# Kernel optimization log

Measured on AMD Instinct MI355X. Metric: run time of the kernel, lower is better.

Reference implementation:

```python
import jax, jax.numpy as jnp
import numpy as np

SIGMA = 2.5
NEIGH_THRESH = 8.0
COORD_SCALE = 40.0  # Angstrom-scale box so the 8A cutoff gives realistic sparsity


def _rbf_weights(vs, vg):
    # vs: [B, Ns, 3], vg: [B, Ng, 3] -> [B, Ns, Ng] row-normalized gaussian RBF
    d2 = (jnp.sum(vs * vs, -1)[:, :, None]
          + jnp.sum(vg * vg, -1)[:, None, :]
          - 2.0 * jnp.einsum('bnd,bmd->bnm', vs, vg))
    d2 = jnp.maximum(d2, 0.0)
    w = jnp.exp(-d2 / (SIGMA ** 2)) * (d2 < NEIGH_THRESH ** 2)
    return w / (jnp.sum(w, -1, keepdims=True) + 1e-8)


def setup_inputs() -> dict:
    key = jax.random.key(0)
    ks = jax.random.split(key, 12)
    B, Ns, Ng, D = 4, 16384, 2048, 128
    s = 1.0 / np.sqrt(D)
    sp = 1.0 / np.sqrt(2 * D)
    return {
        'xs': jax.random.normal(ks[0], (B, Ns, D), jnp.float32),
        'xg': jax.random.normal(ks[1], (B, Ng, D), jnp.float32),
        'vs': jax.random.uniform(ks[2], (B, Ns, 3), jnp.float32) * COORD_SCALE,
        'vg': jax.random.uniform(ks[3], (B, Ng, 3), jnp.float32) * COORD_SCALE,
        'Ws_pre': jax.random.normal(ks[4], (D, D), jnp.float32) * s,
        'bs_pre': jnp.zeros((D,), jnp.float32),
        'Wg_pre': jax.random.normal(ks[5], (D, D), jnp.float32) * s,
        'bg_pre': jnp.zeros((D,), jnp.float32),
        'Ws_post': jax.random.normal(ks[6], (2 * D, D), jnp.float32) * sp,
        'bs_post': jnp.zeros((D,), jnp.float32),
        'Wg_post': jax.random.normal(ks[7], (2 * D, D), jnp.float32) * sp,
        'bg_post': jnp.zeros((D,), jnp.float32),
    }


def reference(xs, xg, vs, vg, Ws_pre, bs_pre, Wg_pre, bg_pre,
              Ws_post, bs_post, Wg_post, bg_post):
    # pre-encoders (surface.x = s_pre_block(surface.x); graph.x = g_pre_block(graph.x))
    xs_h = jax.nn.relu(jnp.einsum('bnd,de->bne', xs, Ws_pre) + bs_pre)
    xg_h = jax.nn.relu(jnp.einsum('bmd,de->bme', xg, Wg_pre) + bg_pre)
    # RBF bipartite message passing (non-BP path): xs_out = rbf_w @ graph.x; xg_out = rbf_w.T @ surface.x
    w = _rbf_weights(vs, vg)                                  # [B, Ns, Ng]
    xs_out = jnp.einsum('bnm,bmd->bnd', w, xg_h)              # graph -> surface
    xg_out = jnp.einsum('bnm,bnd->bmd', w, xs_h)              # surface -> graph
    # post blocks fuse old features with messages
    xs_new = jax.nn.relu(jnp.einsum('bnd,de->bne',
                                    jnp.concatenate([xs_h, xs_out], -1), Ws_post) + bs_post)
    xg_new = jax.nn.relu(jnp.einsum('bmd,de->bme',
                                    jnp.concatenate([xg_h, xg_out], -1), Wg_post) + bg_post)
    # concat along node dim so output is a single array: [B, Ns+Ng, D]
    return jnp.concatenate([xs_new, xg_new], axis=1)
```

## Files before the change

### kernel.cpp

```cpp
#include <hip/hip_runtime.h>
#include <hip/hip_bf16.h>

#define BB 4
#define NS 16384
#define NG 2048
#define DD 128
#define SPLITG 16
#define C2F (-0.23083120f)

typedef short bf16x8 __attribute__((ext_vector_type(8)));
typedef unsigned short u16x8 __attribute__((ext_vector_type(8)));
typedef float f32x4 __attribute__((ext_vector_type(4)));
typedef float f32x16 __attribute__((ext_vector_type(16)));
typedef int i32x4 __attribute__((ext_vector_type(4)));

#if __has_builtin(__builtin_amdgcn_exp2f)
#define EXP2(x) __builtin_amdgcn_exp2f(x)
#else
#define EXP2(x) exp2f(x)
#endif

__device__ __forceinline__ unsigned short f2bf(float x) {
  unsigned int u = __builtin_bit_cast(unsigned int, x);
  u += 0x7FFFu + ((u >> 16) & 1u);
  return (unsigned short)(u >> 16);
}
__device__ __forceinline__ float bf2f(unsigned short h) {
  unsigned int u = ((unsigned int)h) << 16;
  return __builtin_bit_cast(float, u);
}

#define PACK_SWAP(e0, e1, e2, e3, e4, e5, e6, e7, OUT)                        \
  {                                                                           \
    unsigned pq0, pq1, pq2, pq3;                                              \
    asm("v_cvt_pk_bf16_f32 %0, %4, %5\n\t"                                    \
        "v_cvt_pk_bf16_f32 %1, %6, %7\n\t"                                    \
        "v_cvt_pk_bf16_f32 %2, %8, %9\n\t"                                    \
        "v_cvt_pk_bf16_f32 %3, %10, %11\n\t"                                  \
        "s_nop 1\n\t"                                                         \
        "v_permlane32_swap_b32 %0, %2\n\t"                                    \
        "v_permlane32_swap_b32 %1, %3\n\t"                                    \
        "s_nop 1"                                                             \
        : "=&v"(pq0), "=&v"(pq1), "=&v"(pq2), "=&v"(pq3)                      \
        : "v"(e0), "v"(e1), "v"(e2), "v"(e3), "v"(e4), "v"(e5), "v"(e6),      \
          "v"(e7));                                                           \
    i32x4 tmp_ = {(int)pq0, (int)pq1, (int)pq2, (int)pq3};                    \
    OUT = __builtin_bit_cast(bf16x8, tmp_);                                   \
  }

__device__ __forceinline__ void posprep1(const float* __restrict__ v, int i,
                                         unsigned short* __restrict__ pos1,
                                         unsigned short* __restrict__ pos2) {
  float x = v[i * 3 + 0], y = v[i * 3 + 1], z = v[i * 3 + 2];
  unsigned short hx = f2bf(x), hy = f2bf(y), hz = f2bf(z);
  float fx = bf2f(hx), fy = bf2f(hy), fz = bf2f(hz);
  unsigned short lx = f2bf(x - fx), ly = f2bf(y - fy), lz = f2bf(z - fz);
  float n = x * x + y * y + z * z;
  unsigned short nh = f2bf(n);
  unsigned short nl = f2bf(n - bf2f(nh));
  unsigned short m2hx = f2bf(-2.f * fx), m2hy = f2bf(-2.f * fy),
                 m2hz = f2bf(-2.f * fz);
  unsigned short m2lx = f2bf(-2.f * bf2f(lx)), m2ly = f2bf(-2.f * bf2f(ly)),
                 m2lz = f2bf(-2.f * bf2f(lz));
  const unsigned short one = 0x3F80;
  u16x8 a0 = {m2hx, m2hy, m2hz, m2lx, m2ly, m2lz, m2hx, m2hy};
  u16x8 a1 = {m2hz, m2lx, m2ly, m2lz, nh, nl, one, one};
  u16x8 b0 = {hx, hy, hz, hx, hy, hz, lx, ly};
  u16x8 b1 = {lz, lx, ly, lz, one, one, nh, nl};
  *(u16x8*)(pos1 + (long)i * 16) = a0;
  *(u16x8*)(pos1 + (long)i * 16 + 8) = a1;
  *(u16x8*)(pos2 + (long)i * 16) = b0;
  *(u16x8*)(pos2 + (long)i * 16 + 8) = b1;
}

__global__ __launch_bounds__(256) void prep_k(
    const float* __restrict__ vs, const float* __restrict__ vg,
    const float* __restrict__ Ws_pre, const float* __restrict__ Wg_pre,
    const float* __restrict__ Ws_post, const float* __restrict__ Wg_post,
    unsigned short* __restrict__ pos1_s, unsigned short* __restrict__ pos2_s,
    unsigned short* __restrict__ pos1_g, unsigned short* __restrict__ pos2_g,
    unsigned short* __restrict__ WtS_pre, unsigned short* __restrict__ WtG_pre,
    unsigned short* __restrict__ WtS_post,
    unsigned short* __restrict__ WtG_post) {
  const int NODEBLK = (BB * (NS + NG)) / 256;
  int bid = blockIdx.x, tid = threadIdx.x;
  if (bid < NODEBLK) {
    int i = bid * 256 + tid;
    if (i < BB * NS)
      posprep1(vs, i, pos1_s, pos2_s);
    else
      posprep1(vg, i - BB * NS, pos1_g, pos2_g);
  } else {
    int k2 = (bid - NODEBLK) * 256 + tid;
    const float* W;
    unsigned short* Wt;
    int kshift, loc;
    if (k2 < 16384) { W = Ws_pre; Wt = WtS_pre; kshift = 7; loc = k2; }
    else if (k2 < 32768) { W = Wg_pre; Wt = WtG_pre; kshift = 7; loc = k2 - 16384; }
    else if (k2 < 65536) { W = Ws_post; Wt = WtS_post; kshift = 8; loc = k2 - 32768; }
    else { W = Wg_post; Wt = WtG_post; kshift = 8; loc = k2 - 65536; }
    int K = 1 << kshift;
    int e = loc >> kshift, k = loc & (K - 1);
    Wt[(long)e * K + k] = f2bf(W[(long)k * 128 + e]);
  }
}

__global__ __launch_bounds__(256) void pre_mfma_k(
    const float* __restrict__ xs, const float* __restrict__ xg,
    const unsigned short* __restrict__ WtS,
    const unsigned short* __restrict__ WtG, const float* __restrict__ bs,
    const float* __restrict__ bg, unsigned short* __restrict__ xs_h,
    unsigned short* __restrict__ xg_h) {
  long r0 = (long)blockIdx.x * 64;
  const float* X;
  const unsigned short* Wt;
  const float* bias;
  unsigned short* H;
  long row0;
  if (r0 < (long)BB * NS) {
    X = xs; Wt = WtS; bias = bs; H = xs_h; row0 = r0;
  } else {
    X = xg; Wt = WtG; bias = bg; H = xg_h; row0 = r0 - (long)BB * NS;
  }
  int tid = threadIdx.x, l = tid & 63, w = tid >> 6;
  int g = l >> 4, r = l & 15;
  row0 += w * 16;
  const float* xrow = X + (row0 + r) * DD;
  f32x4 z4 = {0.f, 0.f, 0.f, 0.f};
  f32x4 acc[8];
#pragma unroll
  for (int i = 0; i < 8; ++i) acc[i] = z4;
#pragma unroll
  for (int ks = 0; ks < 4; ++ks) {
    float4 v0 = *(const float4*)(xrow + ks * 32 + 8 * g);
    float4 v1 = *(const float4*)(xrow + ks * 32 + 8 * g + 4);
    bf16x8 a;
    a[0] = (short)f2bf(v0.x); a[1] = (short)f2bf(v0.y);
    a[2] = (short)f2bf(v0.z); a[3] = (short)f2bf(v0.w);
    a[4] = (short)f2bf(v1.x); a[5] = (short)f2bf(v1.y);
    a[6] = (short)f2bf(v1.z); a[7] = (short)f2bf(v1.w);
#pragma unroll
    for (int ct = 0; ct < 8; ++ct) {
      bf16x8 b = *reinterpret_cast<const bf16x8*>(Wt + (ct * 16 + r) * DD +
                                                  ks * 32 + 8 * g);
      acc[ct] = __builtin_amdgcn_mfma_f32_16x16x32_bf16(a, b, acc[ct], 0, 0, 0);
    }
  }
#pragma unroll
  for (int ct = 0; ct < 8; ++ct) {
    float bv = bias[ct * 16 + r];
#pragma unroll
    for (int r4 = 0; r4 < 4; ++r4) {
      long row = row0 + 4 * g + r4;
      H[row * DD + ct * 16 + r] = f2bf(fmaxf(acc[ct][r4] + bv, 0.f));
    }
  }
}

__global__ __launch_bounds__(256) void transpose_k(
    const unsigned short* __restrict__ H, unsigned short* __restrict__ HT,
    int R, const float* __restrict__ scale) {
  __shared__ unsigned short lds[64 * 136];
  int tid = threadIdx.x;
  long r0 = (long)blockIdx.x * 64;
#pragma unroll
  for (int q = 0; q < 4; ++q) {
    int idx = q * 2048 + tid * 8;
    int rr = idx >> 7, cc = idx & 127;
    u16x8 v = *reinterpret_cast<const u16x8*>(H + (r0 + rr) * 128 + cc);
    if (scale) {
      float s = scale[r0 + rr];
#pragma unroll
      for (int i = 0; i < 8; ++i) v[i] = f2bf(bf2f(v[i]) * s);
    }
    *(u16x8*)&lds[rr * 136 + cc] = v;
  }
  __syncthreads();
  int e = tid >> 1, half = tid & 1;
#pragma unroll
  for (int q = 0; q < 4; ++q) {
    u16x8 v;
#pragma unroll
    for (int i = 0; i < 8; ++i)
      v[i] = lds[(half * 32 + q * 8 + i) * 136 + e];
    *reinterpret_cast<u16x8*>(HT + (long)e * R + r0 + half * 32 + q * 8) = v;
  }
}

__global__ __launch_bounds__(256) void msg_s_k(
    const unsigned short* __restrict__ pos1_g,
    const unsigned short* __restrict__ pos2_s,
    const unsigned short* __restrict__ xg_hT, unsigned short* __restrict__ xs_o,
    float* __restrict__ rsinv) {
  __shared__ __align__(16) unsigned short ldsB[2][128 * 64];
  const int tid = threadIdx.x;
  const int w = tid >> 6, l = tid & 63;
  const int ln = l & 31, hi = l >> 5;
  const int b = blockIdx.y;
  const long bNS = (long)b * NS, bNG = (long)b * NG;
  const long row0 = (long)blockIdx.x * 128 + w * 32;
  const long BNG = (long)BB * NG;
  const int NCH = NG / 64;

  const bf16x8 bP = *reinterpret_cast<const bf16x8*>(
      pos2_s + (bNS + row0 + ln) * 16 + 8 * hi);

  const f32x16 zz = {0.f, 0.f, 0.f, 0.f, 0.f, 0.f, 0.f, 0.f,
                     0.f, 0.f, 0.f, 0.f, 0.f, 0.f, 0.f, 0.f};
  f32x16 acc[4] = {zz, zz, zz, zz};
  float rs0 = 0.f, rs1 = 0.f, rs2 = 0.f, rs3 = 0.f;

  const int tf = tid >> 3;
  const int tsp = tid & 7;
  const unsigned short* p0 = xg_hT + (long)tf * BNG + bNG + (tsp ^ (tf & 7)) * 8;
  const unsigned short* p1 = p0 + (long)32 * BNG;
  const unsigned short* p2 = p0 + (long)64 * BNG;
  const unsigned short* p3 = p0 + (long)96 * BNG;
  const unsigned short* pp = pos1_g + (bNG + ln) * 16 + 8 * hi;

  u16x8 stA[4];
  bf16x8 pA0, pA1, pA0n, pA1n;
  stA[0] = *reinterpret_cast<const u16x8*>(p0);
  stA[1] = *reinterpret_cast<const u16x8*>(p1);
  stA[2] = *reinterpret_cast<const u16x8*>(p2);
  stA[3] = *reinterpret_cast<const u16x8*>(p3);
#pragma unroll
  for (int q = 0; q < 4; ++q)
    *(u16x8*)&ldsB[0][(q * 32 + tf) * 64 + tsp * 8] = stA[q];
  stA[0] = *reinterpret_cast<const u16x8*>(p0 + 64);
  stA[1] = *reinterpret_cast<const u16x8*>(p1 + 64);
  stA[2] = *reinterpret_cast<const u16x8*>(p2 + 64);
  stA[3] = *reinterpret_cast<const u16x8*>(p3 + 64);
  p0 += 128; p1 += 128; p2 += 128; p3 += 128;
  pA0 = *reinterpret_cast<const bf16x8*>(pp);
  pA1 = *reinterpret_cast<const bf16x8*>(pp + 32 * 16);
  pA0n = *reinterpret_cast<const bf16x8*>(pp + 64 * 16);
  pA1n = *reinterpret_cast<const bf16x8*>(pp + 96 * 16);
  pp += 128 * 16;
  __syncthreads();

#pragma unroll 1
  for (int c = 0; c < NCH; ++c) {
    const int buf = c & 1;
    float ex[2][16];
    bf16x8 fr[2][2];
    f32x16 S0 = __builtin_amdgcn_mfma_f32_32x32x16_bf16(pA0, bP, zz, 0, 0, 0);
    f32x16 S1 = __builtin_amdgcn_mfma_f32_32x32x16_bf16(pA1, bP, zz, 0, 0, 0);
#pragma unroll
    for (int r = 0; r < 16; ++r) ex[0][r] = EXP2(S0[r] * C2F);
    PACK_SWAP(ex[0][0], ex[0][1], ex[0][2], ex[0][3], ex[0][4], ex[0][5],
              ex[0][6], ex[0][7], fr[0][0]);
    PACK_SWAP(ex[0][8], ex[0][9], ex[0][10], ex[0][11], ex[0][12], ex[0][13],
              ex[0][14], ex[0][15], fr[0][1]);
#pragma unroll
    for (int r = 0; r < 16; ++r) ex[1][r] = EXP2(S1[r] * C2F);
    PACK_SWAP(ex[1][0], ex[1][1], ex[1][2], ex[1][3], ex[1][4], ex[1][5],
              ex[1][6], ex[1][7], fr[1][0]);
    PACK_SWAP(ex[1][8], ex[1][9], ex[1][10], ex[1][11], ex[1][12], ex[1][13],
              ex[1][14], ex[1][15], fr[1][1]);
#pragma unroll
    for (int r = 0; r < 4; ++r) {
      rs0 += ex[0][r] + ex[1][r];
      rs1 += ex[0][r + 4] + ex[1][r + 4];
      rs2 += ex[0][r + 8] + ex[1][r + 8];
      rs3 += ex[0][r + 12] + ex[1][r + 12];
    }
#pragma unroll
    for (int t2 = 0; t2 < 2; ++t2) {
#pragma unroll
      for (int kh = 0; kh < 2; ++kh) {
        const int kt = t2 * 2 + kh;
        const int spr = ((kt * 2 + hi) ^ (ln & 7)) * 8;
#pragma unroll
        for (int nt = 0; nt < 4; ++nt) {
          const bf16x8 bm = *reinterpret_cast<const bf16x8*>(
              &ldsB[buf][(nt * 32 + ln) * 64 + spr]);
          acc[nt] = __builtin_amdgcn_mfma_f32_32x32x16_bf16(fr[t2][kh], bm,
                                                            acc[nt], 0, 0, 0);
        }
      }
    }
    if (c + 1 < NCH) {
#pragma unroll
      for (int q = 0; q < 4; ++q)
        *(u16x8*)&ldsB[buf ^ 1][(q * 32 + tf) * 64 + tsp * 8] = stA[q];
    }
    if (c + 2 < NCH) {
      stA[0] = *reinterpret_cast<const u16x8*>(p0);
      stA[1] = *reinterpret_cast<const u16x8*>(p1);
      stA[2] = *reinterpret_cast<const u16x8*>(p2);
      stA[3] = *reinterpret_cast<const u16x8*>(p3);
      p0 += 64; p1 += 64; p2 += 64; p3 += 64;
    }
    pA0 = pA0n;
    pA1 = pA1n;
    if (c + 2 < NCH) {
      pA0n = *reinterpret_cast<const bf16x8*>(pp);
      pA1n = *reinterpret_cast<const bf16x8*>(pp + 32 * 16);
      pp += 64 * 16;
    }
    __syncthreads();
  }

  float rtot = (rs0 + rs1) + (rs2 + rs3);
  rtot += __shfl_xor(rtot, 32, 64);
  float denom = rtot + 1e-8f;
  float rsi = 1.f / denom;
  if (hi == 0) rsinv[bNS + row0 + ln] = rsi;
#pragma unroll
  for (int r = 0; r < 16; ++r) {
    const int crow = (r & 3) + 8 * (r >> 2) + 4 * hi;
    float rsib = __shfl(rsi, crow, 64);
    long rowg = bNS + row0 + crow;
#pragma unroll
    for (int nt = 0; nt < 4; ++nt)
      xs_o[rowg * DD + nt * 32 + ln] = f2bf(acc[nt][r] * rsib);
  }
}

__global__ __launch_bounds__(256) void msg_g_k(
    const unsigned short* __restrict__ pos1_s,
    const unsigned short* __restrict__ pos2_g,
    const unsigned short* __restrict__ xs_hT, unsigned short* __restrict__ part) {
  __shared__ __align__(16) unsigned short ldsB[2][128 * 64];
  const int tid = threadIdx.x;
  const int w = tid >> 6, l = tid & 63;
  const int ln = l & 31, hi = l >> 5;
  const int b = blockIdx.y, spz = blockIdx.z;
  const long bNS = (long)b * NS, bNG = (long)b * NG;
  const long nbeg = (long)spz * (NS / SPLITG);
  const long row0 = (long)blockIdx.x * 128 + w * 32;
  const long BNS = (long)BB * NS;
  const int NCH = (NS / SPLITG) / 64;

  const bf16x8 bP = *reinterpret_cast<const bf16x8*>(
      pos2_g + (bNG + row0 + ln) * 16 + 8 * hi);

  const f32x16 zz = {0.f, 0.f, 0.f, 0.f, 0.f, 0.f, 0.f, 0.f,
                     0.f, 0.f, 0.f, 0.f, 0.f, 0.f, 0.f, 0.f};
  f32x16 acc[4] = {zz, zz, zz, zz};

  const int tf = tid >> 3;
  const int tsp = tid & 7;
  const unsigned short* p0 = xs_hT + (long)tf * BNS + bNS + nbeg +
                             (tsp ^ (tf & 7)) * 8;
  const unsigned short* p1 = p0 + (long)32 * BNS;
  const unsigned short* p2 = p0 + (long)64 * BNS;
  const unsigned short* p3 = p0 + (long)96 * BNS;
  const unsigned short* pp = pos1_s + (bNS + nbeg + ln) * 16 + 8 * hi;

  u16x8 stA[4];
  bf16x8 pA0, pA1, pA0n, pA1n;
  stA[0] = *reinterpret_cast<const u16x8*>(p0);
  stA[1] = *reinterpret_cast<const u16x8*>(p1);
  stA[2] = *reinterpret_cast<const u16x8*>(p2);
  stA[3] = *reinterpret_cast<const u16x8*>(p3);
#pragma unroll
  for (int q = 0; q < 4; ++q)
    *(u16x8*)&ldsB[0][(q * 32 + tf) * 64 + tsp * 8] = stA[q];
  stA[0] = *reinterpret_cast<const u16x8*>(p0 + 64);
  stA[1] = *reinterpret_cast<const u16x8*>(p1 + 64);
  stA[2] = *reinterpret_cast<const u16x8*>(p2 + 64);
  stA[3] = *reinterpret_cast<const u16x8*>(p3 + 64);
  p0 += 128; p1 += 128; p2 += 128; p3 += 128;
  pA0 = *reinterpret_cast<const bf16x8*>(pp);
  pA1 = *reinterpret_cast<const bf16x8*>(pp + 32 * 16);
  pA0n = *reinterpret_cast<const bf16x8*>(pp + 64 * 16);
  pA1n = *reinterpret_cast<const bf16x8*>(pp + 96 * 16);
  pp += 128 * 16;
  __syncthreads();

#pragma unroll 1
  for (int c = 0; c < NCH; ++c) {
    const int buf = c & 1;
    float ex[2][16];
    bf16x8 fr[2][2];
    f32x16 S0 = __builtin_amdgcn_mfma_f32_32x32x16_bf16(pA0, bP, zz, 0, 0, 0);
    f32x16 S1 = __builtin_amdgcn_mfma_f32_32x32x16_bf16(pA1, bP, zz, 0, 0, 0);
#pragma unroll
    for (int r = 0; r < 16; ++r) ex[0][r] = EXP2(S0[r] * C2F);
    PACK_SWAP(ex[0][0], ex[0][1], ex[0][2], ex[0][3], ex[0][4], ex[0][5],
              ex[0][6], ex[0][7], fr[0][0]);
    PACK_SWAP(ex[0][8], ex[0][9], ex[0][10], ex[0][11], ex[0][12], ex[0][13],
              ex[0][14], ex[0][15], fr[0][1]);
#pragma unroll
    for (int r = 0; r < 16; ++r) ex[1][r] = EXP2(S1[r] * C2F);
    PACK_SWAP(ex[1][0], ex[1][1], ex[1][2], ex[1][3], ex[1][4], ex[1][5],
              ex[1][6], ex[1][7], fr[1][0]);
    PACK_SWAP(ex[1][8], ex[1][9], ex[1][10], ex[1][11], ex[1][12], ex[1][13],
              ex[1][14], ex[1][15], fr[1][1]);
#pragma unroll
    for (int t2 = 0; t2 < 2; ++t2) {
#pragma unroll
      for (int kh = 0; kh < 2; ++kh) {
        const int kt = t2 * 2 + kh;
        const int spr = ((kt * 2 + hi) ^ (ln & 7)) * 8;
#pragma unroll
        for (int nt = 0; nt < 4; ++nt) {
          const bf16x8 bm = *reinterpret_cast<const bf16x8*>(
              &ldsB[buf][(nt * 32 + ln) * 64 + spr]);
          acc[nt] = __builtin_amdgcn_mfma_f32_32x32x16_bf16(fr[t2][kh], bm,
                                                            acc[nt], 0, 0, 0);
        }
      }
    }
    if (c + 1 < NCH) {
#pragma unroll
      for (int q = 0; q < 4; ++q)
        *(u16x8*)&ldsB[buf ^ 1][(q * 32 + tf) * 64 + tsp * 8] = stA[q];
    }
    if (c + 2 < NCH) {
      stA[0] = *reinterpret_cast<const u16x8*>(p0);
      stA[1] = *reinterpret_cast<const u16x8*>(p1);
      stA[2] = *reinterpret_cast<const u16x8*>(p2);
      stA[3] = *reinterpret_cast<const u16x8*>(p3);
      p0 += 64; p1 += 64; p2 += 64; p3 += 64;
    }
    pA0 = pA0n;
    pA1 = pA1n;
    if (c + 2 < NCH) {
      pA0n = *reinterpret_cast<const bf16x8*>(pp);
      pA1n = *reinterpret_cast<const bf16x8*>(pp + 32 * 16);
      pp += 64 * 16;
    }
    __syncthreads();
  }

  const long pbase = (long)spz * BB * NG;
#pragma unroll
  for (int r = 0; r < 16; ++r) {
    const int crow = (r & 3) + 8 * (r >> 2) + 4 * hi;
    long rowg = pbase + bNG + row0 + crow;
#pragma unroll
    for (int nt = 0; nt < 4; ++nt)
      part[rowg * DD + nt * 32 + ln] = f2bf(acc[nt][r]);
  }
}

__global__ __launch_bounds__(256) void reduce_k(
    const unsigned short* __restrict__ part, unsigned short* __restrict__ xg_o) {
  long i = ((long)blockIdx.x * 256 + threadIdx.x) * 8;
  const long S = (long)BB * NG * DD;
  float a[8];
#pragma unroll
  for (int k = 0; k < 8; ++k) a[k] = 0.f;
#pragma unroll
  for (int s = 0; s < SPLITG; ++s) {
    u16x8 v = *reinterpret_cast<const u16x8*>(part + s * S + i);
#pragma unroll
    for (int k = 0; k < 8; ++k) a[k] += bf2f(v[k]);
  }
  u16x8 o;
#pragma unroll
  for (int k = 0; k < 8; ++k) o[k] = f2bf(a[k]);
  *reinterpret_cast<u16x8*>(xg_o + i) = o;
}

__global__ __launch_bounds__(256) void post_mfma_k(
    const unsigned short* __restrict__ Ha, const unsigned short* __restrict__ Hb,
    const unsigned short* __restrict__ Wt, const float* __restrict__ bias,
    float* __restrict__ out, int shift, int mask, int off) {
  int tid = threadIdx.x, l = tid & 63, w = tid >> 6;
  int g = l >> 4, r = l & 15;
  long row0 = (long)blockIdx.x * 64 + w * 16;
  const unsigned short* ha = Ha + (row0 + r) * DD;
  const unsigned short* hb = Hb + (row0 + r) * DD;
  f32x4 z4 = {0.f, 0.f, 0.f, 0.f};
  f32x4 acc[8];
#pragma unroll
  for (int i = 0; i < 8; ++i) acc[i] = z4;
#pragma unroll
  for (int ks = 0; ks < 8; ++ks) {
    const unsigned short* src = (ks < 4) ? (ha + ks * 32) : (hb + (ks - 4) * 32);
    bf16x8 a = *reinterpret_cast<const bf16x8*>(src + 8 * g);
#pragma unroll
    for (int ct = 0; ct < 8; ++ct) {
      bf16x8 b = *reinterpret_cast<const bf16x8*>(Wt + (ct * 16 + r) * 256 +
                                                  ks * 32 + 8 * g);
      acc[ct] = __builtin_amdgcn_mfma_f32_16x16x32_bf16(a, b, acc[ct], 0, 0, 0);
    }
  }
#pragma unroll
  for (int ct = 0; ct < 8; ++ct) {
    float bv = bias[ct * 16 + r];
#pragma unroll
    for (int r4 = 0; r4 < 4; ++r4) {
      long rowg = row0 + 4 * g + r4;
      long bb = rowg >> shift;
      long n = rowg & mask;
      out[(bb * (NS + NG) + off + n) * DD + ct * 16 + r] =
          fmaxf(acc[ct][r4] + bv, 0.f);
    }
  }
}

extern "C" void kernel_launch(void* const* d_in, const int* in_sizes, int n_in,
                              void* d_out, int out_size, void* d_ws,
                              size_t ws_size, hipStream_t stream) {
  const float* xs = (const float*)d_in[0];
  const float* xg = (const float*)d_in[1];
  const float* vs = (const float*)d_in[2];
  const float* vg = (const float*)d_in[3];
  const float* Ws_pre = (const float*)d_in[4];
  const float* bs_pre = (const float*)d_in[5];
  const float* Wg_pre = (const float*)d_in[6];
  const float* bg_pre = (const float*)d_in[7];
  const float* Ws_post = (const float*)d_in[8];
  const float* bs_post = (const float*)d_in[9];
  const float* Wg_post = (const float*)d_in[10];
  const float* bg_post = (const float*)d_in[11];
  float* out = (float*)d_out;

  char* p = (char*)d_ws;
  unsigned short* pos1_s = (unsigned short*)p; p += (size_t)BB * NS * 16 * 2;
  unsigned short* pos2_s = (unsigned short*)p; p += (size_t)BB * NS * 16 * 2;
  unsigned short* pos1_g = (unsigned short*)p; p += (size_t)BB * NG * 16 * 2;
  unsigned short* pos2_g = (unsigned short*)p; p += (size_t)BB * NG * 16 * 2;
  unsigned short* WtS_pre = (unsigned short*)p; p += (size_t)128 * 128 * 2;
  unsigned short* WtG_pre = (unsigned short*)p; p += (size_t)128 * 128 * 2;
  unsigned short* WtS_post = (unsigned short*)p; p += (size_t)128 * 256 * 2;
  unsigned short* WtG_post = (unsigned short*)p; p += (size_t)128 * 256 * 2;
  unsigned short* xg_h = (unsigned short*)p; p += (size_t)BB * NG * DD * 2;
  unsigned short* xg_hT = (unsigned short*)p; p += (size_t)BB * NG * DD * 2;
  unsigned short* xs_hT = (unsigned short*)p; p += (size_t)BB * NS * DD * 2;
  unsigned short* xg_o = (unsigned short*)p; p += (size_t)BB * NG * DD * 2;
  float* rsinv = (float*)p; p += (size_t)BB * NS * 4;
  unsigned short* xs_h = (unsigned short*)p;
  unsigned short* xs_o = xs_h + (size_t)BB * NS * DD;
  unsigned short* part_g = xs_h;
  p += (size_t)2 * BB * NS * DD * 2;

  prep_k<<<(BB * (NS + NG)) / 256 + 98304 / 256, 256, 0, stream>>>(
      vs, vg, Ws_pre, Wg_pre, Ws_post, Wg_post, pos1_s, pos2_s, pos1_g,
      pos2_g, WtS_pre, WtG_pre, WtS_post, WtG_post);
  pre_mfma_k<<<(BB * NS + BB * NG) / 64, 256, 0, stream>>>(
      xs, xg, WtS_pre, WtG_pre, bs_pre, bg_pre, xs_h, xg_h);
  transpose_k<<<BB * NG / 64, 256, 0, stream>>>(xg_h, xg_hT, BB * NG, nullptr);
  msg_s_k<<<dim3(NS / 128, BB), 256, 0, stream>>>(pos1_g, pos2_s, xg_hT, xs_o,
                                                  rsinv);
  transpose_k<<<BB * NS / 64, 256, 0, stream>>>(xs_h, xs_hT, BB * NS, rsinv);
  post_mfma_k<<<BB * NS / 64, 256, 0, stream>>>(xs_h, xs_o, WtS_post, bs_post,
                                                out, 14, NS - 1, 0);
  msg_g_k<<<dim3(NG / 128, BB, SPLITG), 256, 0, stream>>>(pos1_s, pos2_g,
                                                          xs_hT, part_g);
  reduce_k<<<(BB * NG * DD) / 8 / 256, 256, 0, stream>>>(part_g, xg_o);
  post_mfma_k<<<BB * NG / 64, 256, 0, stream>>>(xg_h, xg_o, WtG_post, bg_post,
                                                out, 11, NG - 1, NS);
}
```

Before: 204.1 us.

## Precompute row sums and merge both message kernels into one interleaved launch

Computes the RBF row-normalisation sums in a separate column-split rowsum kernel, so the surface-scaled transpose no longer has to wait for the surface message kernel. The graph→surface and surface→graph message GEMMs then run as alternating blocks of one 1024-block launch, giving the GPU a single larger wave of work. The graph-side split-K partials are accumulated with float atomics into a zeroed buffer plus a small convert kernel, replacing the bf16 partial buffer and the reduce kernel. The cost is recomputing the exp tile once more for the row sums, plus atomic traffic and a memset.

```diff
diff --git a/kernel.cpp b/kernel.cpp
--- a/kernel.cpp
+++ b/kernel.cpp
@@ -5,11 +5,13 @@
 #define NS 16384
 #define NG 2048
 #define DD 128
-#define SPLITG 16
+#define SPLITG 8
+#define CSPLIT 4
 #define C2F (-0.23083120f)
 
 typedef short bf16x8 __attribute__((ext_vector_type(8)));
 typedef unsigned short u16x8 __attribute__((ext_vector_type(8)));
+typedef unsigned short u16x4 __attribute__((ext_vector_type(4)));
 typedef float f32x4 __attribute__((ext_vector_type(4)));
 typedef float f32x16 __attribute__((ext_vector_type(16)));
 typedef int i32x4 __attribute__((ext_vector_type(4)));
@@ -157,9 +159,38 @@
   }
 }
 
+__global__ __launch_bounds__(256) void rowsum_k(
+    const unsigned short* __restrict__ pos1_g,
+    const unsigned short* __restrict__ pos2_s, float* __restrict__ rs_part) {
+  const int tid = threadIdx.x;
+  const int w = tid >> 6, l = tid & 63;
+  const int ln = l & 31, hi = l >> 5;
+  const int b = blockIdx.y, cz = blockIdx.z;
+  const long bNS = (long)b * NS, bNG = (long)b * NG;
+  const long row0 = (long)blockIdx.x * 128 + w * 32;
+  const int NCOL = NG / CSPLIT;
+
+  const bf16x8 bP = *reinterpret_cast<const bf16x8*>(
+      pos2_s + (bNS + row0 + ln) * 16 + 8 * hi);
+  const unsigned short* pp =
+      pos1_g + (bNG + (long)cz * NCOL + ln) * 16 + 8 * hi;
+  const f32x16 zz = {0.f, 0.f, 0.f, 0.f, 0.f, 0.f, 0.f, 0.f,
+                     0.f, 0.f, 0.f, 0.f, 0.f, 0.f, 0.f, 0.f};
+  float rsl = 0.f;
+#pragma unroll 2
+  for (int c = 0; c < NCOL / 32; ++c) {
+    bf16x8 a = *reinterpret_cast<const bf16x8*>(pp + (long)c * 32 * 16);
+    f32x16 S = __builtin_amdgcn_mfma_f32_32x32x16_bf16(a, bP, zz, 0, 0, 0);
+#pragma unroll
+    for (int r = 0; r < 16; ++r) rsl += EXP2(S[r] * C2F);
+  }
+  rsl += __shfl_xor(rsl, 32, 64);
+  if (hi == 0) rs_part[(long)cz * (BB * NS) + bNS + row0 + ln] = rsl;
+}
+
 __global__ __launch_bounds__(256) void transpose_k(
     const unsigned short* __restrict__ H, unsigned short* __restrict__ HT,
-    int R, const float* __restrict__ scale) {
+    int R, const float* __restrict__ rsp, float* __restrict__ rsinv_out) {
   __shared__ unsigned short lds[64 * 136];
   int tid = threadIdx.x;
   long r0 = (long)blockIdx.x * 64;
@@ -168,10 +199,14 @@
     int idx = q * 2048 + tid * 8;
     int rr = idx >> 7, cc = idx & 127;
     u16x8 v = *reinterpret_cast<const u16x8*>(H + (r0 + rr) * 128 + cc);
-    if (scale) {
-      float s = scale[r0 + rr];
-#pragma unroll
-      for (int i = 0; i < 8; ++i) v[i] = f2bf(bf2f(v[i]) * s);
+    if (rsp) {
+      long row = r0 + rr;
+      float s = rsp[row] + rsp[(long)BB * NS + row] +
+                rsp[2L * BB * NS + row] + rsp[3L * BB * NS + row] + 1e-8f;
+      float ri = 1.f / s;
+#pragma unroll
+      for (int i = 0; i < 8; ++i) v[i] = f2bf(bf2f(v[i]) * ri);
+      if (cc == 0) rsinv_out[row] = ri;
     }
     *(u16x8*)&lds[rr * 136 + cc] = v;
   }
@@ -187,273 +222,249 @@
   }
 }
 
-__global__ __launch_bounds__(256) void msg_s_k(
+__global__ __launch_bounds__(256) void msg_merged_k(
     const unsigned short* __restrict__ pos1_g,
     const unsigned short* __restrict__ pos2_s,
-    const unsigned short* __restrict__ xg_hT, unsigned short* __restrict__ xs_o,
-    float* __restrict__ rsinv) {
+    const unsigned short* __restrict__ xg_hT,
+    const unsigned short* __restrict__ pos1_s,
+    const unsigned short* __restrict__ pos2_g,
+    const unsigned short* __restrict__ xs_hT,
+    const float* __restrict__ rsinv, unsigned short* __restrict__ xs_o,
+    float* __restrict__ xg_acc) {
   __shared__ __align__(16) unsigned short ldsB[2][128 * 64];
   const int tid = threadIdx.x;
   const int w = tid >> 6, l = tid & 63;
   const int ln = l & 31, hi = l >> 5;
-  const int b = blockIdx.y;
-  const long bNS = (long)b * NS, bNG = (long)b * NG;
-  const long row0 = (long)blockIdx.x * 128 + w * 32;
-  const long BNG = (long)BB * NG;
-  const int NCH = NG / 64;
-
-  const bf16x8 bP = *reinterpret_cast<const bf16x8*>(
-      pos2_s + (bNS + row0 + ln) * 16 + 8 * hi);
-
+  const int bid = blockIdx.x;
+  const int role = bid & 1;
+  const int idx = bid >> 1;
   const f32x16 zz = {0.f, 0.f, 0.f, 0.f, 0.f, 0.f, 0.f, 0.f,
                      0.f, 0.f, 0.f, 0.f, 0.f, 0.f, 0.f, 0.f};
-  f32x16 acc[4] = {zz, zz, zz, zz};
-  float rs0 = 0.f, rs1 = 0.f, rs2 = 0.f, rs3 = 0.f;
-
   const int tf = tid >> 3;
   const int tsp = tid & 7;
-  const unsigned short* p0 = xg_hT + (long)tf * BNG + bNG + (tsp ^ (tf & 7)) * 8;
-  const unsigned short* p1 = p0 + (long)32 * BNG;
-  const unsigned short* p2 = p0 + (long)64 * BNG;
-  const unsigned short* p3 = p0 + (long)96 * BNG;
-  const unsigned short* pp = pos1_g + (bNG + ln) * 16 + 8 * hi;
-
-  u16x8 stA[4];
-  bf16x8 pA0, pA1, pA0n, pA1n;
-  stA[0] = *reinterpret_cast<const u16x8*>(p0);
-  stA[1] = *reinterpret_cast<const u16x8*>(p1);
-  stA[2] = *reinterpret_cast<const u16x8*>(p2);
-  stA[3] = *reinterpret_cast<const u16x8*>(p3);
-#pragma unroll
-  for (int q = 0; q < 4; ++q)
-    *(u16x8*)&ldsB[0][(q * 32 + tf) * 64 + tsp * 8] = stA[q];
-  stA[0] = *reinterpret_cast<const u16x8*>(p0 + 64);
-  stA[1] = *reinterpret_cast<const u16x8*>(p1 + 64);
-  stA[2] = *reinterpret_cast<const u16x8*>(p2 + 64);
-  stA[3] = *reinterpret_cast<const u16x8*>(p3 + 64);
-  p0 += 128; p1 += 128; p2 += 128; p3 += 128;
-  pA0 = *reinterpret_cast<const bf16x8*>(pp);
-  pA1 = *reinterpret_cast<const bf16x8*>(pp + 32 * 16);
-  pA0n = *reinterpret_cast<const bf16x8*>(pp + 64 * 16);
-  pA1n = *reinterpret_cast<const bf16x8*>(pp + 96 * 16);
-  pp += 128 * 16;
-  __syncthreads();
+
+  if (role == 0) {
+    const int b = idx >> 7;
+    const long bNS = (long)b * NS, bNG = (long)b * NG;
+    const long row0 = (long)(idx & 127) * 128 + w * 32;
+    const long BNG = (long)BB * NG;
+    const int NCH = NG / 64;
+
+    const bf16x8 bP = *reinterpret_cast<const bf16x8*>(
+        pos2_s + (bNS + row0 + ln) * 16 + 8 * hi);
+    f32x16 acc[4] = {zz, zz, zz, zz};
+
+    const unsigned short* p0 =
+        xg_hT + (long)tf * BNG + bNG + (tsp ^ (tf & 7)) * 8;
+    const unsigned short* p1 = p0 + (long)32 * BNG;
+    const unsigned short* p2 = p0 + (long)64 * BNG;
+    const unsigned short* p3 = p0 + (long)96 * BNG;
+    const unsigned short* pp = pos1_g + (bNG + ln) * 16 + 8 * hi;
+
+    u16x8 stA[4];
+    bf16x8 pA0, pA1, pA0n, pA1n;
+    stA[0] = *reinterpret_cast<const u16x8*>(p0);
+    stA[1] = *reinterpret_cast<const u16x8*>(p1);
+    stA[2] = *reinterpret_cast<const u16x8*>(p2);
+    stA[3] = *reinterpret_cast<const u16x8*>(p3);
+#pragma unroll
+    for (int q = 0; q < 4; ++q)
+      *(u16x8*)&ldsB[0][(q * 32 + tf) * 64 + tsp * 8] = stA[q];
+    stA[0] = *reinterpret_cast<const u16x8*>(p0 + 64);
+    stA[1] = *reinterpret_cast<const u16x8*>(p1 + 64);
+    stA[2] = *reinterpret_cast<const u16x8*>(p2 + 64);
+    stA[3] = *reinterpret_cast<const u16x8*>(p3 + 64);
+    p0 += 128; p1 += 128; p2 += 128; p3 += 128;
+    pA0 = *reinterpret_cast<const bf16x8*>(pp);
+    pA1 = *reinterpret_cast<const bf16x8*>(pp + 32 * 16);
+    pA0n = *reinterpret_cast<const bf16x8*>(pp + 64 * 16);
+    pA1n = *reinterpret_cast<const bf16x8*>(pp + 96 * 16);
+    pp += 128 * 16;
+    __syncthreads();
 
 #pragma unroll 1
-  for (int c = 0; c < NCH; ++c) {
-    const int buf = c & 1;
-    float ex[2][16];
-    bf16x8 fr[2][2];
-    f32x16 S0 = __builtin_amdgcn_mfma_f32_32x32x16_bf16(pA0, bP, zz, 0, 0, 0);
-    f32x16 S1 = __builtin_amdgcn_mfma_f32_32x32x16_bf16(pA1, bP, zz, 0, 0, 0);
-#pragma unroll
-    for (int r = 0; r < 16; ++r) ex[0][r] = EXP2(S0[r] * C2F);
-    PACK_SWAP(ex[0][0], ex[0][1], ex[0][2], ex[0][3], ex[0][4], ex[0][5],
-              ex[0][6], ex[0][7], fr[0][0]);
-    PACK_SWAP(ex[0][8], ex[0][9], ex[0][10], ex[0][11], ex[0][12], ex[0][13],
-              ex[0][14], ex[0][15], fr[0][1]);
-#pragma unroll
-    for (int r = 0; r < 16; ++r) ex[1][r] = EXP2(S1[r] * C2F);
-    PACK_SWAP(ex[1][0], ex[1][1], ex[1][2], ex[1][3], ex[1][4], ex[1][5],
-              ex[1][6], ex[1][7], fr[1][0]);
-    PACK_SWAP(ex[1][8], ex[1][9], ex[1][10], ex[1][11], ex[1][12], ex[1][13],
-              ex[1][14], ex[1][15], fr[1][1]);
-#pragma unroll
-    for (int r = 0; r < 4; ++r) {
-      rs0 += ex[0][r] + ex[1][r];
-      rs1 += ex[0][r + 4] + ex[1][r + 4];
-      rs2 += ex[0][r + 8] + ex[1][r + 8];
-      rs3 += ex[0][r + 12] + ex[1][r + 12];
-    }
-#pragma unroll
-    for (int t2 = 0; t2 < 2; ++t2) {
-#pragma unroll
-      for (int kh = 0; kh < 2; ++kh) {
-        const int kt = t2 * 2 + kh;
-        const int spr = ((kt * 2 + hi) ^ (ln & 7)) * 8;
-#pragma unroll
-        for (int nt = 0; nt < 4; ++nt) {
-          const bf16x8 bm = *reinterpret_cast<const bf16x8*>(
-              &ldsB[buf][(nt * 32 + ln) * 64 + spr]);
-          acc[nt] = __builtin_amdgcn_mfma_f32_32x32x16_bf16(fr[t2][kh], bm,
-                                                            acc[nt], 0, 0, 0);
+    for (int c = 0; c < NCH; ++c) {
+      const int buf = c & 1;
+      float ex[2][16];
+      bf16x8 fr[2][2];
+      f32x16 S0 = __builtin_amdgcn_mfma_f32_32x32x16_bf16(pA0, bP, zz, 0, 0, 0);
+      f32x16 S1 = __builtin_amdgcn_mfma_f32_32x32x16_bf16(pA1, bP, zz, 0, 0, 0);
+#pragma unroll
+      for (int r = 0; r < 16; ++r) ex[0][r] = EXP2(S0[r] * C2F);
+      PACK_SWAP(ex[0][0], ex[0][1], ex[0][2], ex[0][3], ex[0][4], ex[0][5],
+                ex[0][6], ex[0][7], fr[0][0]);
+      PACK_SWAP(ex[0][8], ex[0][9], ex[0][10], ex[0][11], ex[0][12], ex[0][13],
+                ex[0][14], ex[0][15], fr[0][1]);
+#pragma unroll
+      for (int r = 0; r < 16; ++r) ex[1][r] = EXP2(S1[r] * C2F);
+      PACK_SWAP(ex[1][0], ex[1][1], ex[1][2], ex[1][3], ex[1][4], ex[1][5],
+                ex[1][6], ex[1][7], fr[1][0]);
+      PACK_SWAP(ex[1][8], ex[1][9], ex[1][10], ex[1][11], ex[1][12], ex[1][13],
+                ex[1][14], ex[1][15], fr[1][1]);
+#pragma unroll
+      for (int t2 = 0; t2 < 2; ++t2) {
+#pragma unroll
+        for (int kh = 0; kh < 2; ++kh) {
+          const int kt = t2 * 2 + kh;
+          const int spr = ((kt * 2 + hi) ^ (ln & 7)) * 8;
+#pragma unroll
+          for (int nt = 0; nt < 4; ++nt) {
+            const bf16x8 bm = *reinterpret_cast<const bf16x8*>(
+                &ldsB[buf][(nt * 32 + ln) * 64 + spr]);
+            acc[nt] = __builtin_amdgcn_mfma_f32_32x32x16_bf16(fr[t2][kh], bm,
+                                                              acc[nt], 0, 0, 0);
+          }
         }
       }
-    }
-    if (c + 1 < NCH) {
-#pragma unroll
-      for (int q = 0; q < 4; ++q)
-        *(u16x8*)&ldsB[buf ^ 1][(q * 32 + tf) * 64 + tsp * 8] = stA[q];
-    }
-    if (c + 2 < NCH) {
-      stA[0] = *reinterpret_cast<const u16x8*>(p0);
-      stA[1] = *reinterpret_cast<const u16x8*>(p1);
-      stA[2] = *reinterpret_cast<const u16x8*>(p2);
-      stA[3] = *reinterpret_cast<const u16x8*>(p3);
-      p0 += 64; p1 += 64; p2 += 64; p3 += 64;
-    }
-    pA0 = pA0n;
-    pA1 = pA1n;
-    if (c + 2 < NCH) {
-      pA0n = *reinterpret_cast<const bf16x8*>(pp);
-      pA1n = *reinterpret_cast<const bf16x8*>(pp + 32 * 16);
-      pp += 64 * 16;
-    }
+      if (c + 1 < NCH) {
+#pragma unroll
+        for (int q = 0; q < 4; ++q)
+          *(u16x8*)&ldsB[buf ^ 1][(q * 32 + tf) * 64 + tsp * 8] = stA[q];
+      }
+      if (c + 2 < NCH) {
+        stA[0] = *reinterpret_cast<const u16x8*>(p0);
+        stA[1] = *reinterpret_cast<const u16x8*>(p1);
+        stA[2] = *reinterpret_cast<const u16x8*>(p2);
+        stA[3] = *reinterpret_cast<const u16x8*>(p3);
+        p0 += 64; p1 += 64; p2 += 64; p3 += 64;
+      }
+      pA0 = pA0n;
+      pA1 = pA1n;
+      if (c + 2 < NCH) {
+        pA0n = *reinterpret_cast<const bf16x8*>(pp);
+        pA1n = *reinterpret_cast<const bf16x8*>(pp + 32 * 16);
+        pp += 64 * 16;
+      }
+      __syncthreads();
+    }
+
+    float rsi = rsinv[bNS + row0 + ln];
+#pragma unroll
+    for (int r = 0; r < 16; ++r) {
+      const int crow = (r & 3) + 8 * (r >> 2) + 4 * hi;
+      float rsib = __shfl(rsi, crow, 64);
+      long rowg = bNS + row0 + crow;
+#pragma unroll
+      for (int nt = 0; nt < 4; ++nt)
+        xs_o[rowg * DD + nt * 32 + ln] = f2bf(acc[nt][r] * rsib);
+    }
+  } else {
+    const int gx = idx & 15;
+    const int b = (idx >> 4) & 3;
+    const int spz = idx >> 6;
+    const long bNS = (long)b * NS, bNG = (long)b * NG;
+    const long nbeg = (long)spz * (NS / SPLITG);
+    const long row0 = (long)gx * 128 + w * 32;
+    const long BNS = (long)BB * NS;
+    const int NCH = (NS / SPLITG) / 64;
+
+    const bf16x8 bP = *reinterpret_cast<const bf16x8*>(
+        pos2_g + (bNG + row0 + ln) * 16 + 8 * hi);
+    f32x16 acc[4] = {zz, zz, zz, zz};
+
+    const unsigned short* p0 =
+        xs_hT + (long)tf * BNS + bNS + nbeg + (tsp ^ (tf & 7)) * 8;
+    const unsigned short* p1 = p0 + (long)32 * BNS;
+    const unsigned short* p2 = p0 + (long)64 * BNS;
+    const unsigned short* p3 = p0 + (long)96 * BNS;
+    const unsigned short* pp = pos1_s + (bNS + nbeg + ln) * 16 + 8 * hi;
+
+    u16x8 stA[4];
+    bf16x8 pA0, pA1, pA0n, pA1n;
+    stA[0] = *reinterpret_cast<const u16x8*>(p0);
+    stA[1] = *reinterpret_cast<const u16x8*>(p1);
+    stA[2] = *reinterpret_cast<const u16x8*>(p2);
+    stA[3] = *reinterpret_cast<const u16x8*>(p3);
+#pragma unroll
+    for (int q = 0; q < 4; ++q)
+      *(u16x8*)&ldsB[0][(q * 32 + tf) * 64 + tsp * 8] = stA[q];
+    stA[0] = *reinterpret_cast<const u16x8*>(p0 + 64);
+    stA[1] = *reinterpret_cast<const u16x8*>(p1 + 64);
+    stA[2] = *reinterpret_cast<const u16x8*>(p2 + 64);
+    stA[3] = *reinterpret_cast<const u16x8*>(p3 + 64);
+    p0 += 128; p1 += 128; p2 += 128; p3 += 128;
+    pA0 = *reinterpret_cast<const bf16x8*>(pp);
+    pA1 = *reinterpret_cast<const bf16x8*>(pp + 32 * 16);
+    pA0n = *reinterpret_cast<const bf16x8*>(pp + 64 * 16);
+    pA1n = *reinterpret_cast<const bf16x8*>(pp + 96 * 16);
+    pp += 128 * 16;
     __syncthreads();
-  }
-
-  float rtot = (rs0 + rs1) + (rs2 + rs3);
-  rtot += __shfl_xor(rtot, 32, 64);
-  float denom = rtot + 1e-8f;
-  float rsi = 1.f / denom;
-  if (hi == 0) rsinv[bNS + row0 + ln] = rsi;
-#pragma unroll
-  for (int r = 0; r < 16; ++r) {
-    const int crow = (r & 3) + 8 * (r >> 2) + 4 * hi;
-    float rsib = __shfl(rsi, crow, 64);
-    long rowg = bNS + row0 + crow;
-#pragma unroll
-    for (int nt = 0; nt < 4; ++nt)
-      xs_o[rowg * DD + nt * 32 + ln] = f2bf(acc[nt][r] * rsib);
-  }
-}
-
-__global__ __launch_bounds__(256) void msg_g_k(
-    const unsigned short* __restrict__ pos1_s,
-    const unsigned short* __restrict__ pos2_g,
-    const unsigned short* __restrict__ xs_hT, unsigned short* __restrict__ part) {
-  __shared__ __align__(16) unsigned short ldsB[2][128 * 64];
-  const int tid = threadIdx.x;
-  const int w = tid >> 6, l = tid & 63;
-  const int ln = l & 31, hi = l >> 5;
-  const int b = blockIdx.y, spz = blockIdx.z;
-  const long bNS = (long)b * NS, bNG = (long)b * NG;
-  const long nbeg = (long)spz * (NS / SPLITG);
-  const long row0 = (long)blockIdx.x * 128 + w * 32;
-  const long BNS = (long)BB * NS;
-  const int NCH = (NS / SPLITG) / 64;
-
-  const bf16x8 bP = *reinterpret_cast<const bf16x8*>(
-      pos2_g + (bNG + row0 + ln) * 16 + 8 * hi);
-
-  const f32x16 zz = {0.f, 0.f, 0.f, 0.f, 0.f, 0.f, 0.f, 0.f,
-                     0.f, 0.f, 0.f, 0.f, 0.f, 0.f, 0.f, 0.f};
-  f32x16 acc[4] = {zz, zz, zz, zz};
-
-  const int tf = tid >> 3;
-  const int tsp = tid & 7;
-  const unsigned short* p0 = xs_hT + (long)tf * BNS + bNS + nbeg +
-                             (tsp ^ (tf & 7)) * 8;
-  const unsigned short* p1 = p0 + (long)32 * BNS;
-  const unsigned short* p2 = p0 + (long)64 * BNS;
-  const unsigned short* p3 = p0 + (long)96 * BNS;
-  const unsigned short* pp = pos1_s + (bNS + nbeg + ln) * 16 + 8 * hi;
-
-  u16x8 stA[4];
-  bf16x8 pA0, pA1, pA0n, pA1n;
-  stA[0] = *reinterpret_cast<const u16x8*>(p0);
-  stA[1] = *reinterpret_cast<const u16x8*>(p1);
-  stA[2] = *reinterpret_cast<const u16x8*>(p2);
-  stA[3] = *reinterpret_cast<const u16x8*>(p3);
-#pragma unroll
-  for (int q = 0; q < 4; ++q)
-    *(u16x8*)&ldsB[0][(q * 32 + tf) * 64 + tsp * 8] = stA[q];
-  stA[0] = *reinterpret_cast<const u16x8*>(p0 + 64);
-  stA[1] = *reinterpret_cast<const u16x8*>(p1 + 64);
-  stA[2] = *reinterpret_cast<const u16x8*>(p2 + 64);
-  stA[3] = *reinterpret_cast<const u16x8*>(p3 + 64);
-  p0 += 128; p1 += 128; p2 += 128; p3 += 128;
-  pA0 = *reinterpret_cast<const bf16x8*>(pp);
-  pA1 = *reinterpret_cast<const bf16x8*>(pp + 32 * 16);
-  pA0n = *reinterpret_cast<const bf16x8*>(pp + 64 * 16);
-  pA1n = *reinterpret_cast<const bf16x8*>(pp + 96 * 16);
-  pp += 128 * 16;
-  __syncthreads();
 
 #pragma unroll 1
-  for (int c = 0; c < NCH; ++c) {
-    const int buf = c & 1;
-    float ex[2][16];
-    bf16x8 fr[2][2];
-    f32x16 S0 = __builtin_amdgcn_mfma_f32_32x32x16_bf16(pA0, bP, zz, 0, 0, 0);
-    f32x16 S1 = __builtin_amdgcn_mfma_f32_32x32x16_bf16(pA1, bP, zz, 0, 0, 0);
-#pragma unroll
-    for (int r = 0; r < 16; ++r) ex[0][r] = EXP2(S0[r] * C2F);
-    PACK_SWAP(ex[0][0], ex[0][1], ex[0][2], ex[0][3], ex[0][4], ex[0][5],
-              ex[0][6], ex[0][7], fr[0][0]);
-    PACK_SWAP(ex[0][8], ex[0][9], ex[0][10], ex[0][11], ex[0][12], ex[0][13],
-              ex[0][14], ex[0][15], fr[0][1]);
-#pragma unroll
-    for (int r = 0; r < 16; ++r) ex[1][r] = EXP2(S1[r] * C2F);
-    PACK_SWAP(ex[1][0], ex[1][1], ex[1][2], ex[1][3], ex[1][4], ex[1][5],
-              ex[1][6], ex[1][7], fr[1][0]);
-    PACK_SWAP(ex[1][8], ex[1][9], ex[1][10], ex[1][11], ex[1][12], ex[1][13],
-              ex[1][14], ex[1][15], fr[1][1]);
-#pragma unroll
-    for (int t2 = 0; t2 < 2; ++t2) {
-#pragma unroll
-      for (int kh = 0; kh < 2; ++kh) {
-        const int kt = t2 * 2 + kh;
-        const int spr = ((kt * 2 + hi) ^ (ln & 7)) * 8;
-#pragma unroll
-        for (int nt = 0; nt < 4; ++nt) {
-          const bf16x8 bm = *reinterpret_cast<const bf16x8*>(
-              &ldsB[buf][(nt * 32 + ln) * 64 + spr]);
-          acc[nt] = __builtin_amdgcn_mfma_f32_32x32x16_bf16(fr[t2][kh], bm,
-                                                            acc[nt], 0, 0, 0);
+    for (int c = 0; c < NCH; ++c) {
+      const int buf = c & 1;
+      float ex[2][16];
+      bf16x8 fr[2][2];
+      f32x16 S0 = __builtin_amdgcn_mfma_f32_32x32x16_bf16(pA0, bP, zz, 0, 0, 0);
+      f32x16 S1 = __builtin_amdgcn_mfma_f32_32x32x16_bf16(pA1, bP, zz, 0, 0, 0);
+#pragma unroll
+      for (int r = 0; r < 16; ++r) ex[0][r] = EXP2(S0[r] * C2F);
+      PACK_SWAP(ex[0][0], ex[0][1], ex[0][2], ex[0][3], ex[0][4], ex[0][5],
+                ex[0][6], ex[0][7], fr[0][0]);
+      PACK_SWAP(ex[0][8], ex[0][9], ex[0][10], ex[0][11], ex[0][12], ex[0][13],
+                ex[0][14], ex[0][15], fr[0][1]);
+#pragma unroll
+      for (int r = 0; r < 16; ++r) ex[1][r] = EXP2(S1[r] * C2F);
+      PACK_SWAP(ex[1][0], ex[1][1], ex[1][2], ex[1][3], ex[1][4], ex[1][5],
+                ex[1][6], ex[1][7], fr[1][0]);
+      PACK_SWAP(ex[1][8], ex[1][9], ex[1][10], ex[1][11], ex[1][12], ex[1][13],
+                ex[1][14], ex[1][15], fr[1][1]);
+#pragma unroll
+      for (int t2 = 0; t2 < 2; ++t2) {
+#pragma unroll
+        for (int kh = 0; kh < 2; ++kh) {
+          const int kt = t2 * 2 + kh;
+          const int spr = ((kt * 2 + hi) ^ (ln & 7)) * 8;
+#pragma unroll
+          for (int nt = 0; nt < 4; ++nt) {
+            const bf16x8 bm = *reinterpret_cast<const bf16x8*>(
+                &ldsB[buf][(nt * 32 + ln) * 64 + spr]);
+            acc[nt] = __builtin_amdgcn_mfma_f32_32x32x16_bf16(fr[t2][kh], bm,
+                                                              acc[nt], 0, 0, 0);
+          }
         }
       }
-    }
-    if (c + 1 < NCH) {
-#pragma unroll
-      for (int q = 0; q < 4; ++q)
-        *(u16x8*)&ldsB[buf ^ 1][(q * 32 + tf) * 64 + tsp * 8] = stA[q];
-    }
-    if (c + 2 < NCH) {
-      stA[0] = *reinterpret_cast<const u16x8*>(p0);
-      stA[1] = *reinterpret_cast<const u16x8*>(p1);
-      stA[2] = *reinterpret_cast<const u16x8*>(p2);
-      stA[3] = *reinterpret_cast<const u16x8*>(p3);
-      p0 += 64; p1 += 64; p2 += 64; p3 += 64;
-    }
-    pA0 = pA0n;
-    pA1 = pA1n;
-    if (c + 2 < NCH) {
-      pA0n = *reinterpret_cast<const bf16x8*>(pp);
-      pA1n = *reinterpret_cast<const bf16x8*>(pp + 32 * 16);
-      pp += 64 * 16;
-    }
-    __syncthreads();
-  }
-
-  const long pbase = (long)spz * BB * NG;
-#pragma unroll
-  for (int r = 0; r < 16; ++r) {
-    const int crow = (r & 3) + 8 * (r >> 2) + 4 * hi;
-    long rowg = pbase + bNG + row0 + crow;
-#pragma unroll
-    for (int nt = 0; nt < 4; ++nt)
-      part[rowg * DD + nt * 32 + ln] = f2bf(acc[nt][r]);
-  }
-}
-
-__global__ __launch_bounds__(256) void reduce_k(
-    const unsigned short* __restrict__ part, unsigned short* __restrict__ xg_o) {
-  long i = ((long)blockIdx.x * 256 + threadIdx.x) * 8;
-  const long S = (long)BB * NG * DD;
-  float a[8];
-#pragma unroll
-  for (int k = 0; k < 8; ++k) a[k] = 0.f;
-#pragma unroll
-  for (int s = 0; s < SPLITG; ++s) {
-    u16x8 v = *reinterpret_cast<const u16x8*>(part + s * S + i);
-#pragma unroll
-    for (int k = 0; k < 8; ++k) a[k] += bf2f(v[k]);
-  }
-  u16x8 o;
-#pragma unroll
-  for (int k = 0; k < 8; ++k) o[k] = f2bf(a[k]);
-  *reinterpret_cast<u16x8*>(xg_o + i) = o;
+      if (c + 1 < NCH) {
+#pragma unroll
+        for (int q = 0; q < 4; ++q)
+          *(u16x8*)&ldsB[buf ^ 1][(q * 32 + tf) * 64 + tsp * 8] = stA[q];
+      }
+      if (c + 2 < NCH) {
+        stA[0] = *reinterpret_cast<const u16x8*>(p0);
+        stA[1] = *reinterpret_cast<const u16x8*>(p1);
+        stA[2] = *reinterpret_cast<const u16x8*>(p2);
+        stA[3] = *reinterpret_cast<const u16x8*>(p3);
+        p0 += 64; p1 += 64; p2 += 64; p3 += 64;
+      }
+      pA0 = pA0n;
+      pA1 = pA1n;
+      if (c + 2 < NCH) {
+        pA0n = *reinterpret_cast<const bf16x8*>(pp);
+        pA1n = *reinterpret_cast<const bf16x8*>(pp + 32 * 16);
+        pp += 64 * 16;
+      }
+      __syncthreads();
+    }
+
+#pragma unroll
+    for (int r = 0; r < 16; ++r) {
+      const int crow = (r & 3) + 8 * (r >> 2) + 4 * hi;
+      long rowg = bNG + row0 + crow;
+#pragma unroll
+      for (int nt = 0; nt < 4; ++nt)
+        atomicAdd(&xg_acc[rowg * DD + nt * 32 + ln], acc[nt][r]);
+    }
+  }
+}
+
+__global__ __launch_bounds__(256) void convert_k(
+    const float* __restrict__ xg_acc, unsigned short* __restrict__ xg_o) {
+  long i = ((long)blockIdx.x * 256 + threadIdx.x) * 4;
+  f32x4 v = *reinterpret_cast<const f32x4*>(xg_acc + i);
+  u16x4 o;
+#pragma unroll
+  for (int k = 0; k < 4; ++k) o[k] = f2bf(v[k]);
+  *reinterpret_cast<u16x4*>(xg_o + i) = o;
 }
 
 __global__ __launch_bounds__(256) void post_mfma_k(
@@ -525,25 +536,28 @@
   unsigned short* xs_hT = (unsigned short*)p; p += (size_t)BB * NS * DD * 2;
   unsigned short* xg_o = (unsigned short*)p; p += (size_t)BB * NG * DD * 2;
   float* rsinv = (float*)p; p += (size_t)BB * NS * 4;
-  unsigned short* xs_h = (unsigned short*)p;
-  unsigned short* xs_o = xs_h + (size_t)BB * NS * DD;
-  unsigned short* part_g = xs_h;
-  p += (size_t)2 * BB * NS * DD * 2;
+  float* rs_part = (float*)p; p += (size_t)CSPLIT * BB * NS * 4;
+  float* xg_acc = (float*)p; p += (size_t)BB * NG * DD * 4;
+  unsigned short* xs_h = (unsigned short*)p; p += (size_t)BB * NS * DD * 2;
+  unsigned short* xs_o = (unsigned short*)p; p += (size_t)BB * NS * DD * 2;
 
   prep_k<<<(BB * (NS + NG)) / 256 + 98304 / 256, 256, 0, stream>>>(
       vs, vg, Ws_pre, Wg_pre, Ws_post, Wg_post, pos1_s, pos2_s, pos1_g,
       pos2_g, WtS_pre, WtG_pre, WtS_post, WtG_post);
   pre_mfma_k<<<(BB * NS + BB * NG) / 64, 256, 0, stream>>>(
       xs, xg, WtS_pre, WtG_pre, bs_pre, bg_pre, xs_h, xg_h);
-  transpose_k<<<BB * NG / 64, 256, 0, stream>>>(xg_h, xg_hT, BB * NG, nullptr);
-  msg_s_k<<<dim3(NS / 128, BB), 256, 0, stream>>>(pos1_g, pos2_s, xg_hT, xs_o,
-                                                  rsinv);
-  transpose_k<<<BB * NS / 64, 256, 0, stream>>>(xs_h, xs_hT, BB * NS, rsinv);
+  rowsum_k<<<dim3(NS / 128, BB, CSPLIT), 256, 0, stream>>>(pos1_g, pos2_s,
+                                                           rs_part);
+  transpose_k<<<BB * NG / 64, 256, 0, stream>>>(xg_h, xg_hT, BB * NG, nullptr,
+                                                nullptr);
+  transpose_k<<<BB * NS / 64, 256, 0, stream>>>(xs_h, xs_hT, BB * NS, rs_part,
+                                                rsinv);
+  hipMemsetAsync(xg_acc, 0, (size_t)BB * NG * DD * 4, stream);
+  msg_merged_k<<<1024, 256, 0, stream>>>(pos1_g, pos2_s, xg_hT, pos1_s,
+                                         pos2_g, xs_hT, rsinv, xs_o, xg_acc);
   post_mfma_k<<<BB * NS / 64, 256, 0, stream>>>(xs_h, xs_o, WtS_post, bs_post,
                                                 out, 14, NS - 1, 0);
-  msg_g_k<<<dim3(NG / 128, BB, SPLITG), 256, 0, stream>>>(pos1_s, pos2_g,
-                                                          xs_hT, part_g);
-  reduce_k<<<(BB * NG * DD) / 8 / 256, 256, 0, stream>>>(part_g, xg_o);
+  convert_k<<<(BB * NG * DD) / 4 / 256, 256, 0, stream>>>(xg_acc, xg_o);
   post_mfma_k<<<BB * NG / 64, 256, 0, stream>>>(xg_h, xg_o, WtG_post, bg_post,
                                                 out, 11, NG - 1, NS);
 }
```

Result: slower. 230.7 us (+13.0%).
